# Kernel optimization log

Hardware: AMD Instinct MI355X
Metric: run time of the kernel (lower is better)

Reference implementation:

```python
import jax, jax.numpy as jnp
import numpy as np

N_NODES = 100000
N_EDGES = 1600000
D_FEAT = 64
EPS_NORM = 1e-12  # torch F.normalize clamp


def setup_inputs() -> dict:
    key = jax.random.key(0)
    k1, k2, k3, k4 = jax.random.split(key, 4)
    x = jax.random.normal(k1, (N_NODES, D_FEAT), dtype=jnp.float32)
    row = jax.random.randint(k2, (N_EDGES,), 0, N_NODES, dtype=jnp.int32)
    offset = jax.random.randint(k3, (N_EDGES,), 1, N_NODES, dtype=jnp.int32)
    col = (row + offset) % N_NODES  # guarantees no self-loops
    edge_index = jnp.stack([row, col], axis=0)
    edge_attr = jax.random.uniform(k4, (N_EDGES,), dtype=jnp.float32)  # co-occurrence rates >= 0
    eps = jnp.zeros((1,), dtype=jnp.float32)
    beta = jnp.ones((1,), dtype=jnp.float32)
    return {"x": x, "edge_index": edge_index, "edge_attr": edge_attr, "eps": eps, "beta": beta}


def reference(x, edge_index, edge_attr, eps, beta):
    N, F = x.shape
    row, col = edge_index[0], edge_index[1]

    # Per-source-node L2 normalization of edge_attr (vectorized form of the
    # original python loop: edge_attr[row==i] = normalize(edge_attr[row==i], p=2))
    sq = jax.ops.segment_sum(edge_attr * edge_attr, row, num_segments=N)
    src_norm = jnp.maximum(jnp.sqrt(sq), EPS_NORM)
    ea = edge_attr / src_norm[row]

    # Add self loops with edge_attr = 1
    loop = jnp.arange(N, dtype=row.dtype)
    row2 = jnp.concatenate([row, loop])
    col2 = jnp.concatenate([col, loop])
    ea2 = jnp.concatenate([ea, jnp.ones((N,), dtype=ea.dtype)])

    # Row-wise L2 normalize node features
    xnorm = jnp.maximum(jnp.linalg.norm(x, axis=-1, keepdims=True), EPS_NORM)
    xn = x / xnorm

    # Segment softmax over edges grouped by source node (row)
    alpha = beta[0] * ea2
    amax = jax.ops.segment_max(alpha, row2, num_segments=N)
    e = jnp.exp(alpha - amax[row2])
    denom = jax.ops.segment_sum(e, row2, num_segments=N)
    alpha = e / denom[row2]

    # spmm: out[i] = sum_{(i,j) in E} alpha_ij * xn[j]
    out = jax.ops.segment_sum(alpha[:, None] * xn[col2], row2, num_segments=N)
    return (1.0 + eps[0]) * xn + out
```

## Files before the change

kernel.cpp:

```cpp
#include <hip/hip_runtime.h>
#include <math.h>

#define D 64
#define EPSN 1e-12f
#define RPB1 64
#define RPB1_SH 6
#define NBK_MAX 2048
#define CAPB 1280
#define CH 4096
#define EAQ 511.0f

__device__ __forceinline__ float bf2f(unsigned short u) {
    return __uint_as_float((unsigned)u << 16);
}
__device__ __forceinline__ unsigned short f2bf(float f) {
    unsigned u = __float_as_uint(f);
    u = (u + 0x7FFFu + ((u >> 16) & 1u)) >> 16;
    return (unsigned short)u;
}

__global__ __launch_bounds__(512) void k_xnp1(const int* __restrict__ row,
                                              const int* __restrict__ col,
                                              const float* __restrict__ ea,
                                              int* __restrict__ gcur1,
                                              unsigned* __restrict__ p1,
                                              const float4* __restrict__ x4,
                                              ushort4* __restrict__ xnh4,
                                              int E, int N, int p1b, int NBK1) {
    __shared__ unsigned hist[NBK_MAX];
    __shared__ unsigned gb[NBK_MAX];
    __shared__ unsigned spk[CH];
    __shared__ unsigned short sbk[CH];

    int tid = threadIdx.x;
    if ((int)blockIdx.x < p1b) {
        int base = blockIdx.x * CH;
        int cnt  = min(CH, E - base);

        for (int i = tid; i < NBK_MAX; i += 512) hist[i] = 0;
        __syncthreads();

        for (int j = tid; j < cnt; j += 512) {
            unsigned r = (unsigned)row[base + j];
            unsigned c = (unsigned)col[base + j];
            float    a = ea[base + j];
            unsigned b = r >> RPB1_SH;
            atomicAdd(&hist[b], 1u);
            unsigned q = __float2uint_rn(a * EAQ);
            spk[j] = (q << 23) | ((r & (RPB1 - 1)) << 17) | c;
            sbk[j] = (unsigned short)b;
        }
        __syncthreads();

        for (int i = tid; i < NBK1; i += 512) {
            unsigned c = hist[i];
            if (c) gb[i] = (unsigned)(i * CAPB)
                         + (unsigned)atomicAdd(&gcur1[i], (int)c) - c;
        }
        __syncthreads();

        for (int j = tid; j < cnt; j += 512) {
            unsigned b = sbk[j];
            unsigned gpos = gb[b] + atomicAdd(&hist[b], 1u);
            p1[gpos] = spk[j];
        }
    } else {
        int t = (blockIdx.x - p1b) * 512 + tid;
        int r = t >> 4;
        int g = t & 15;
        if (r >= N) return;
        float4 v = x4[(size_t)r * 16 + g];
        float s = v.x * v.x + v.y * v.y + v.z * v.z + v.w * v.w;
        #pragma unroll
        for (int off = 8; off; off >>= 1) s += __shfl_xor(s, off);
        float inv = 1.0f / fmaxf(sqrtf(s), EPSN);
        ushort4 o;
        o.x = f2bf(v.x * inv); o.y = f2bf(v.y * inv);
        o.z = f2bf(v.z * inv); o.w = f2bf(v.w * inv);
        xnh4[(size_t)r * 16 + g] = o;
    }
}

template <int U>
__device__ __forceinline__ void gstep(const float2* __restrict__ lsrt, int k, unsigned lb,
                                      const char* __restrict__ xb,
                                      float& esum, float& acc) {
    float2 e[U];
    float xv[U];
    #pragma unroll
    for (int u = 0; u < U; ++u) e[u] = lsrt[k + u];
    #pragma unroll
    for (int u = 0; u < U; ++u)
        xv[u] = bf2f(*(const unsigned short*)(xb + (__float_as_uint(e[u].y) + lb)));
    #pragma unroll
    for (int u = 0; u < U; ++u) {
        esum += e[u].x;
        acc = fmaf(e[u].x, xv[u], acc);
    }
}

__global__ __launch_bounds__(512) void k_p2f(const int* __restrict__ gcnt,
                                             const unsigned* __restrict__ p1,
                                             const unsigned short* __restrict__ xnh,
                                             const float* __restrict__ beta,
                                             const float* __restrict__ eps,
                                             float* __restrict__ out, int N) {
    __shared__ float2   lsrt[CAPB];
    __shared__ unsigned lpack[RPB1];
    __shared__ unsigned ldeg[RPB1];
    __shared__ unsigned loff[RPB1];
    __shared__ unsigned lcur[RPB1];
    __shared__ float    lbinv[RPB1];

    int b = blockIdx.x;
    int rowbase = b << RPB1_SH;
    int nrows = min(RPB1, N - rowbase);
    if (nrows <= 0) return;
    int s = b * CAPB;
    int cnt = gcnt[b];
    int tid = threadIdx.x;
    int wv = tid >> 6, lane = tid & 63;
    const char* xb = (const char*)xnh;
    unsigned lb = (unsigned)lane << 1;
    const float DQ = 1.0f / EAQ;

    int grme = rowbase + (wv << 3);

    if (tid < RPB1) lpack[tid] = 0;
    __syncthreads();

    for (int j = tid; j < cnt; j += 512) {
        unsigned pk = p1[s + j];
        unsigned rl = (pk >> 17) & (RPB1 - 1);
        float a = (float)(pk >> 23) * DQ;
        unsigned q = __float2uint_rn(a * a * 32768.0f);
        atomicAdd(&lpack[rl], 0x400000u + q);
    }
    __syncthreads();

    unsigned dv = 0;
    if (tid < RPB1) {
        unsigned pk = lpack[tid];
        dv = pk >> 22;
        ldeg[tid] = dv;
        float sq = (float)(pk & 0x3FFFFFu) * (1.0f / 32768.0f);
        lbinv[tid] = beta[0] / fmaxf(sqrtf(sq), EPSN);
        loff[tid] = dv;
    }
    __syncthreads();
    for (int off = 1; off < RPB1; off <<= 1) {
        unsigned add = (tid < RPB1 && tid >= off) ? loff[tid - off] : 0;
        __syncthreads();
        if (tid < RPB1) loff[tid] += add;
        __syncthreads();
    }
    if (tid < RPB1) {
        unsigned ex = loff[tid] - dv;
        loff[tid] = ex;
        lcur[tid] = ex;
    }
    __syncthreads();

    for (int j = tid; j < cnt; j += 512) {
        unsigned pk = p1[s + j];
        unsigned rl = (pk >> 17) & (RPB1 - 1);
        float a = (float)(pk >> 23) * DQ;
        float w = __expf(a * lbinv[rl]);
        unsigned pos = atomicAdd(&lcur[rl], 1u);
        lsrt[pos] = make_float2(w, __uint_as_float((pk & 0x1FFFFu) << 7));
    }
    __syncthreads();

    float ebv = __expf(beta[0]);
    float c1 = 1.0f + eps[0];
    for (int r = wv; r < nrows; r += 8) {
        int gr = rowbase + r;
        float xs = bf2f(*(const unsigned short*)(xb + (((unsigned)gr << 7) + lb)));
        int ks = (int)loff[r];
        int ke = ks + (int)ldeg[r];
        float esum = 0.0f, acc = 0.0f;
        int k = ks;
        for (; k + 16 <= ke; k += 16) gstep<16>(lsrt, k, lb, xb, esum, acc);
        if (k + 8 <= ke) { gstep<8>(lsrt, k, lb, xb, esum, acc); k += 8; }
        if (k + 4 <= ke) { gstep<4>(lsrt, k, lb, xb, esum, acc); k += 4; }
        for (; k < ke; ++k) {
            float2 e0 = lsrt[k];
            esum += e0.x;
            acc = fmaf(e0.x, bf2f(*(const unsigned short*)(xb + (__float_as_uint(e0.y) + lb))), acc);
        }
        float invden = 1.0f / (esum + ebv);
        out[((size_t)gr << 6) + lane] = c1 * xs + (acc + ebv * xs) * invden;
    }
}

static inline size_t align_up(size_t v, size_t a) { return (v + a - 1) & ~(a - 1); }

extern "C" void kernel_launch(void* const* d_in, const int* in_sizes, int n_in,
                              void* d_out, int out_size, void* d_ws, size_t ws_size,
                              hipStream_t stream) {
    const float* x    = (const float*)d_in[0];
    const int*   ei   = (const int*)d_in[1];
    const float* ea   = (const float*)d_in[2];
    const float* eps  = (const float*)d_in[3];
    const float* beta = (const float*)d_in[4];
    float* out = (float*)d_out;

    int N = in_sizes[0] / D;
    int E = in_sizes[2];
    const int* row = ei;
    const int* col = ei + E;
    int NBK1 = (N + RPB1 - 1) >> RPB1_SH;

    char* base = (char*)d_ws;
    size_t off = 0;
    unsigned short* xnh = (unsigned short*)(base + off); off = align_up(off + (size_t)N * D * sizeof(unsigned short), 256);
    int*      gcur1     = (int*)(base + off);            off = align_up(off + NBK_MAX * sizeof(int), 256);
    unsigned* p1buf     = (unsigned*)(base + off);

    hipMemsetAsync(gcur1, 0, NBK_MAX * sizeof(int), stream);

    int p1_blocks = (E + CH - 1) / CH;
    int xn_blocks = ((size_t)N * 16 + 511) / 512;

    k_xnp1<<<p1_blocks + xn_blocks, 512, 0, stream>>>(row, col, ea, gcur1, p1buf,
                                                      (const float4*)x, (ushort4*)xnh,
                                                      E, N, p1_blocks, NBK1);
    k_p2f <<<NBK1, 512, 0, stream>>>(gcur1, p1buf, xnh, beta, eps, out, N);
}
```

Measured before the change: 76.71 us.

## Split per-bucket global counters into sub-buckets and use wave-shuffle prefix scan

Each row bucket's global cursor is split into 8 sub-bucket cursors, selected by block index. This spreads the global atomics across more addresses and lets each wave in the second kernel read its own fixed-capacity sub-bucket. The multi-barrier shared-memory prefix scan is replaced by a single-wave shuffle scan, and the memset is replaced by a small zeroing kernel. Entries beyond a sub-bucket's capacity are silently dropped, which adds a correctness risk if the edge distribution is skewed.

New measurement: 81.93 us. 6.8% more time.

```diff
diff --git a/kernel.cpp b/kernel.cpp
--- a/kernel.cpp
+++ b/kernel.cpp
@@ -5,8 +5,9 @@
 #define EPSN 1e-12f
 #define RPB1 64
 #define RPB1_SH 6
-#define NBK_MAX 2048
-#define CAPB 1280
+#define NSUB 8
+#define CAPS_SUB 224
+#define CAPB (NSUB * CAPS_SUB)
 #define CH 4096
 #define EAQ 511.0f
 
@@ -19,16 +20,21 @@
     return (unsigned short)u;
 }
 
+__global__ void k_zero(int* __restrict__ g, int n) {
+    int i = blockIdx.x * blockDim.x + threadIdx.x;
+    if (i < n) g[i] = 0;
+}
+
 __global__ __launch_bounds__(512) void k_xnp1(const int* __restrict__ row,
                                               const int* __restrict__ col,
                                               const float* __restrict__ ea,
-                                              int* __restrict__ gcur1,
+                                              int* __restrict__ gcur,
                                               unsigned* __restrict__ p1,
                                               const float4* __restrict__ x4,
                                               ushort4* __restrict__ xnh4,
                                               int E, int N, int p1b, int NBK1) {
-    __shared__ unsigned hist[NBK_MAX];
-    __shared__ unsigned gb[NBK_MAX];
+    __shared__ unsigned hist[2048];
+    __shared__ unsigned gb[2048];
     __shared__ unsigned spk[CH];
     __shared__ unsigned short sbk[CH];
 
@@ -36,8 +42,9 @@
     if ((int)blockIdx.x < p1b) {
         int base = blockIdx.x * CH;
         int cnt  = min(CH, E - base);
-
-        for (int i = tid; i < NBK_MAX; i += 512) hist[i] = 0;
+        int sub  = blockIdx.x & (NSUB - 1);
+
+        for (int i = tid; i < 2048; i += 512) hist[i] = 0;
         __syncthreads();
 
         for (int j = tid; j < cnt; j += 512) {
@@ -54,15 +61,16 @@
 
         for (int i = tid; i < NBK1; i += 512) {
             unsigned c = hist[i];
-            if (c) gb[i] = (unsigned)(i * CAPB)
-                         + (unsigned)atomicAdd(&gcur1[i], (int)c) - c;
+            if (c) gb[i] = (unsigned)((i * NSUB + sub) * CAPS_SUB)
+                         + (unsigned)atomicAdd(&gcur[i * NSUB + sub], (int)c) - c;
         }
         __syncthreads();
 
         for (int j = tid; j < cnt; j += 512) {
             unsigned b = sbk[j];
             unsigned gpos = gb[b] + atomicAdd(&hist[b], 1u);
-            p1[gpos] = spk[j];
+            unsigned lim  = (unsigned)((b * NSUB + (blockIdx.x & (NSUB - 1))) * CAPS_SUB) + CAPS_SUB;
+            if (gpos < lim) p1[gpos] = spk[j];
         }
     } else {
         int t = (blockIdx.x - p1b) * 512 + tid;
@@ -116,21 +124,20 @@
     int rowbase = b << RPB1_SH;
     int nrows = min(RPB1, N - rowbase);
     if (nrows <= 0) return;
-    int s = b * CAPB;
-    int cnt = gcnt[b];
     int tid = threadIdx.x;
     int wv = tid >> 6, lane = tid & 63;
     const char* xb = (const char*)xnh;
     unsigned lb = (unsigned)lane << 1;
     const float DQ = 1.0f / EAQ;
 
-    int grme = rowbase + (wv << 3);
+    int sbase = (b * NSUB + wv) * CAPS_SUB;
+    int scnt  = min(gcnt[b * NSUB + wv], CAPS_SUB);
 
     if (tid < RPB1) lpack[tid] = 0;
     __syncthreads();
 
-    for (int j = tid; j < cnt; j += 512) {
-        unsigned pk = p1[s + j];
+    for (int j = lane; j < scnt; j += 64) {
+        unsigned pk = p1[sbase + j];
         unsigned rl = (pk >> 17) & (RPB1 - 1);
         float a = (float)(pk >> 23) * DQ;
         unsigned q = __float2uint_rn(a * a * 32768.0f);
@@ -138,31 +145,26 @@
     }
     __syncthreads();
 
-    unsigned dv = 0;
-    if (tid < RPB1) {
-        unsigned pk = lpack[tid];
-        dv = pk >> 22;
-        ldeg[tid] = dv;
+    if (wv == 0) {
+        unsigned pk = lpack[lane];
+        unsigned dv = pk >> 22;
+        ldeg[lane] = dv;
         float sq = (float)(pk & 0x3FFFFFu) * (1.0f / 32768.0f);
-        lbinv[tid] = beta[0] / fmaxf(sqrtf(sq), EPSN);
-        loff[tid] = dv;
-    }
-    __syncthreads();
-    for (int off = 1; off < RPB1; off <<= 1) {
-        unsigned add = (tid < RPB1 && tid >= off) ? loff[tid - off] : 0;
-        __syncthreads();
-        if (tid < RPB1) loff[tid] += add;
-        __syncthreads();
-    }
-    if (tid < RPB1) {
-        unsigned ex = loff[tid] - dv;
-        loff[tid] = ex;
-        lcur[tid] = ex;
-    }
-    __syncthreads();
-
-    for (int j = tid; j < cnt; j += 512) {
-        unsigned pk = p1[s + j];
+        lbinv[lane] = beta[0] / fmaxf(sqrtf(sq), EPSN);
+        unsigned val = dv;
+        #pragma unroll
+        for (int off = 1; off < 64; off <<= 1) {
+            unsigned t = __shfl_up(val, off);
+            if (lane >= off) val += t;
+        }
+        unsigned ex = val - dv;
+        loff[lane] = ex;
+        lcur[lane] = ex;
+    }
+    __syncthreads();
+
+    for (int j = lane; j < scnt; j += 64) {
+        unsigned pk = p1[sbase + j];
         unsigned rl = (pk >> 17) & (RPB1 - 1);
         float a = (float)(pk >> 23) * DQ;
         float w = __expf(a * lbinv[rl]);
@@ -210,20 +212,20 @@
     const int* row = ei;
     const int* col = ei + E;
     int NBK1 = (N + RPB1 - 1) >> RPB1_SH;
+    int ncur = NBK1 * NSUB;
 
     char* base = (char*)d_ws;
     size_t off = 0;
     unsigned short* xnh = (unsigned short*)(base + off); off = align_up(off + (size_t)N * D * sizeof(unsigned short), 256);
-    int*      gcur1     = (int*)(base + off);            off = align_up(off + NBK_MAX * sizeof(int), 256);
+    int*      gcur      = (int*)(base + off);            off = align_up(off + (size_t)ncur * sizeof(int), 256);
     unsigned* p1buf     = (unsigned*)(base + off);
-
-    hipMemsetAsync(gcur1, 0, NBK_MAX * sizeof(int), stream);
 
     int p1_blocks = (E + CH - 1) / CH;
     int xn_blocks = ((size_t)N * 16 + 511) / 512;
 
-    k_xnp1<<<p1_blocks + xn_blocks, 512, 0, stream>>>(row, col, ea, gcur1, p1buf,
-                                                      (const float4*)x, (ushort4*)xnh,
-                                                      E, N, p1_blocks, NBK1);
-    k_p2f <<<NBK1, 512, 0, stream>>>(gcur1, p1buf, xnh, beta, eps, out, N);
-}
+    k_zero <<<(ncur + 511) / 512, 512, 0, stream>>>(gcur, ncur);
+    k_xnp1 <<<p1_blocks + xn_blocks, 512, 0, stream>>>(row, col, ea, gcur, p1buf,
+                                                       (const float4*)x, (ushort4*)xnh,
+                                                       E, N, p1_blocks, NBK1);
+    k_p2f  <<<NBK1, 512, 0, stream>>>(gcur, p1buf, xnh, beta, eps, out, N);
+}
```
